# Performance work log

Measured on AMD Instinct MI355X. Metric: run time of the kernel, lower is better.

## Reference

```python
import jax, jax.numpy as jnp
import numpy as np

# convDU3 with stride=1: the torch module loops over height, slicing each row to
# an [n, c, 1, w] tensor and running Conv2d(kernel=(9,1), padding=(4,0)) + ReLU,
# then concatenating rows back along height. Because each per-row input has
# height 1 and is zero-padded to height 9, only the CENTER kernel tap W[:,:,4,0]
# multiplies real data; all other taps multiply zeros. Hence the module is
# mathematically identical to a 1x1 conv with W[:,:,4,0] + bias, then ReLU,
# applied to the full [n, c, h, w] map. We implement that fused form.

CENTER_TAP = 4  # (kernel_h - 1) // 2 for kernel_h = 9


def setup_inputs() -> dict:
    key = jax.random.key(0)
    k1, k2, k3 = jax.random.split(key, 3)
    n, c_in, h, w = 16, 2048, 32, 32
    c_out = 512
    fea = jax.random.normal(k1, (n, c_in, h, w), dtype=jnp.float32)
    # Conv2d weight [out, in, kh, kw] with kaiming-ish scale
    W = jax.random.normal(k2, (c_out, c_in, 9, 1), dtype=jnp.float32) * (1.0 / np.sqrt(c_in * 9))
    b = jax.random.normal(k3, (c_out,), dtype=jnp.float32) * 0.01
    return {"fea": fea, "W": W, "b": b}


def reference(fea, W, b):
    # Only the center tap of the (9,1) kernel contributes (zero padding elsewhere).
    Wc = W[:, :, CENTER_TAP, 0]                      # [c_out, c_in]
    out = jnp.einsum('nchw,oc->nohw', fea, Wc)       # 1x1-conv GEMM
    out = out + b[None, :, None, None]
    return jax.nn.relu(out)
```

## Files before the change

### kernel.cpp

```cpp
#include <hip/hip_runtime.h>

#define C_IN   2048
#define HWSZ   1024
#define NBATCH 16
#define C_OUT  512
#define BM 128
#define BN 128
#define BK 64
#define NKSTEP (C_IN/BK)

typedef __attribute__((ext_vector_type(4))) float f32x4;
typedef __attribute__((ext_vector_type(8))) short bf16x8;

__device__ __forceinline__ unsigned short f2bf(float x){
  unsigned int u = __float_as_uint(x);
  u += 0x7fffu + ((u >> 16) & 1u);
  return (unsigned short)(u >> 16);
}

__global__ void prep_w_kernel(const float* __restrict__ W,
                              unsigned short* __restrict__ Wh){
  int i = blockIdx.x * 256 + threadIdx.x;
  Wh[i] = f2bf(W[(size_t)i * 9 + 4]);
}

union FragU { bf16x8 v; uint4 q; };

__global__ __launch_bounds__(256, 2) void gemm_kernel(
    const float* __restrict__ fea,
    const unsigned short* __restrict__ Wh,
    const float* __restrict__ bias,
    float* __restrict__ out)
{
  __shared__ unsigned short Ah[BM*BK];
  __shared__ unsigned short Bh[BN*BK];
  __shared__ float bias_s[BM];

  const int t   = threadIdx.x;
  const int l   = t & 63;
  const int wid = t >> 6;

  const int bx  = blockIdx.x;
  const int xcd = bx & 7;
  const int s_  = bx >> 3;
  const int mt  = s_ & 3;
  const int pl  = xcd * 16 + (s_ >> 2);
  const int pt  = pl & 7;
  const int nb  = pl >> 3;

  if (t < BM) bias_s[t] = bias[mt*BM + t];

  const unsigned short* whg = Wh + (size_t)mt*BM*C_IN;
  const float* fg = fea + (size_t)nb*C_IN*HWSZ + (size_t)pt*BN;

  const int wr0 = t >> 2;
  const int wh4 = t & 3;
  const int cb  = t >> 5;
  const int pb  = t & 31;

  f32x4 acc[4][4];
  #pragma unroll
  for (int i=0;i<4;i++)
    #pragma unroll
    for (int j=0;j<4;j++) acc[i][j] = (f32x4)0.0f;

  uint4 wv[2][2];
  f32x4 fv[8];

  #pragma unroll
  for (int i=0;i<2;i++)
    #pragma unroll
    for (int h=0;h<2;h++)
      wv[i][h] = *(const uint4*)(whg + (size_t)(wr0 + i*64)*C_IN + h*32 + wh4*8);
  #pragma unroll
  for (int i=0;i<8;i++)
    fv[i] = *(const f32x4*)(fg + (size_t)(cb*8 + i)*HWSZ + pb*4);

  const int fr    = l & 15;
  const int o2    = l >> 4;
  const int mrow0 = (wid >> 1) * 64;
  const int ncol0 = (wid & 1) * 64;

  for (int ks = 0; ks < NKSTEP; ks++){
    __syncthreads();
    #pragma unroll
    for (int i=0;i<2;i++){
      const int r   = wr0 + i*64;
      const int key = (r & 7) << 1;
      #pragma unroll
      for (int h=0;h<2;h++){
        const int q0 = h*8 + wh4*2;
        *(uint4*)&Ah[r*BK + ((q0 ^ key))*4] = wv[i][h];
      }
    }
    {
      unsigned short hb[8][4];
      #pragma unroll
      for (int i=0;i<8;i++)
        #pragma unroll
        for (int j=0;j<4;j++) hb[i][j] = f2bf(fv[i][j]);
      #pragma unroll
      for (int j=0;j<4;j++){
        const int p   = pb*4 + j;
        const int key = (p & 7) << 1;
        uint4 v;
        v.x = (unsigned)hb[0][j] | ((unsigned)hb[1][j] << 16);
        v.y = (unsigned)hb[2][j] | ((unsigned)hb[3][j] << 16);
        v.z = (unsigned)hb[4][j] | ((unsigned)hb[5][j] << 16);
        v.w = (unsigned)hb[6][j] | ((unsigned)hb[7][j] << 16);
        *(uint4*)&Bh[p*BK + (((2*cb) ^ key))*4] = v;
      }
    }
    __syncthreads();

    if (ks + 1 < NKSTEP){
      const int c0 = (ks + 1) * BK;
      #pragma unroll
      for (int i=0;i<2;i++)
        #pragma unroll
        for (int h=0;h<2;h++)
          wv[i][h] = *(const uint4*)(whg + (size_t)(wr0 + i*64)*C_IN + c0 + h*32 + wh4*8);
      #pragma unroll
      for (int i=0;i<8;i++)
        fv[i] = *(const f32x4*)(fg + (size_t)(c0 + cb*8 + i)*HWSZ + pb*4);
    }

    FragU af[4][2], bff[4][2];
    #pragma unroll
    for (int mf=0; mf<4; mf++){
      const int r   = mrow0 + mf*16 + fr;
      const int key = (r & 7) << 1;
      #pragma unroll
      for (int s=0; s<2; s++)
        af[mf][s].q = *(const uint4*)&Ah[r*BK + (((s*8 + 2*o2) ^ key))*4];
    }
    #pragma unroll
    for (int nf=0; nf<4; nf++){
      const int p   = ncol0 + nf*16 + fr;
      const int key = (p & 7) << 1;
      #pragma unroll
      for (int s=0; s<2; s++)
        bff[nf][s].q = *(const uint4*)&Bh[p*BK + (((s*8 + 2*o2) ^ key))*4];
    }

    #pragma unroll
    for (int mf=0; mf<4; mf++)
      #pragma unroll
      for (int nf=0; nf<4; nf++)
        #pragma unroll
        for (int s=0; s<2; s++)
          acc[mf][nf] = __builtin_amdgcn_mfma_f32_16x16x32_bf16(af[mf][s].v, bff[nf][s].v, acc[mf][nf], 0, 0, 0);
  }

  float* ob = out + ((size_t)nb*C_OUT + mt*BM) * HWSZ + (size_t)pt*BN;
  #pragma unroll
  for (int mf=0; mf<4; mf++){
    #pragma unroll
    for (int nf=0; nf<4; nf++){
      const int p = ncol0 + nf*16 + fr;
      #pragma unroll
      for (int rr=0; rr<4; rr++){
        const int o = mrow0 + mf*16 + o2*4 + rr;
        float x = acc[mf][nf][rr] + bias_s[o];
        x = fmaxf(x, 0.0f);
        ob[(size_t)o*HWSZ + p] = x;
      }
    }
  }
}

extern "C" void kernel_launch(void* const* d_in, const int* in_sizes, int n_in,
                              void* d_out, int out_size, void* d_ws, size_t ws_size,
                              hipStream_t stream){
  const float* fea = (const float*)d_in[0];
  const float* W   = (const float*)d_in[1];
  const float* b   = (const float*)d_in[2];
  float* out = (float*)d_out;
  unsigned short* Wh = (unsigned short*)d_ws;
  prep_w_kernel<<<dim3((C_OUT*C_IN)/256), dim3(256), 0, stream>>>(W, Wh);
  gemm_kernel<<<dim3(4*8*NBATCH), dim3(256), 0, stream>>>(fea, Wh, b, out);
}
```

Measured before the change: 306.8 us.

## Pre-swizzle weights into MFMA fragment order and load A directly from global

The weight-prep kernel now writes the bf16 center-tap weights in MFMA fragment order, so each wave loads its A fragments straight from global memory with coalesced 16-byte loads instead of staging them through LDS. The GEMM block shrinks to 128 threads with a 128x64 tile, and the B tile in LDS is double-buffered so only one barrier per k-step is needed. This removes the A-side LDS writes and reads and one sync per step, at the cost of twice as many blocks, each rereading the full weight slice from L2, and fewer waves per block to hide latency.

```diff
diff --git a/kernel.cpp b/kernel.cpp
--- a/kernel.cpp
+++ b/kernel.cpp
@@ -4,9 +4,7 @@
 #define HWSZ   1024
 #define NBATCH 16
 #define C_OUT  512
-#define BM 128
-#define BN 128
-#define BK 64
+#define BK     64
 #define NKSTEP (C_IN/BK)
 
 typedef __attribute__((ext_vector_type(4))) float f32x4;
@@ -18,23 +16,38 @@
   return (unsigned short)(u >> 16);
 }
 
+union FU { bf16x8 v; uint4 q; };
+
 __global__ void prep_w_kernel(const float* __restrict__ W,
-                              unsigned short* __restrict__ Wh){
-  int i = blockIdx.x * 256 + threadIdx.x;
-  Wh[i] = f2bf(W[(size_t)i * 9 + 4]);
+                              unsigned short* __restrict__ Wf){
+  const int tid  = blockIdx.x*256 + threadIdx.x;
+  const int l    = tid & 63;
+  const int frag = tid >> 6;
+  const int mfs  = frag & 7;
+  const int ks   = (frag >> 3) & 31;
+  const int wr   = (frag >> 8) & 1;
+  const int mt   = frag >> 9;
+  const int o    = mt*128 + wr*64 + (mfs>>1)*16 + (l & 15);
+  const int c0   = ks*BK + (mfs & 1)*32 + (l>>4)*8;
+  unsigned short v[8];
+  #pragma unroll
+  for (int j=0;j<8;j++)
+    v[j] = f2bf(W[((size_t)o*C_IN + (size_t)(c0 + j))*9 + 4]);
+  uint4 pk;
+  pk.x = (unsigned)v[0] | ((unsigned)v[1] << 16);
+  pk.y = (unsigned)v[2] | ((unsigned)v[3] << 16);
+  pk.z = (unsigned)v[4] | ((unsigned)v[5] << 16);
+  pk.w = (unsigned)v[6] | ((unsigned)v[7] << 16);
+  *(uint4*)(Wf + (size_t)tid*8) = pk;
 }
 
-union FragU { bf16x8 v; uint4 q; };
-
-__global__ __launch_bounds__(256, 2) void gemm_kernel(
+__global__ __launch_bounds__(128, 2) void gemm_kernel(
     const float* __restrict__ fea,
-    const unsigned short* __restrict__ Wh,
+    const unsigned short* __restrict__ Wf,
     const float* __restrict__ bias,
     float* __restrict__ out)
 {
-  __shared__ unsigned short Ah[BM*BK];
-  __shared__ unsigned short Bh[BN*BK];
-  __shared__ float bias_s[BM];
+  __shared__ unsigned short Bs[2][64*64];
 
   const int t   = threadIdx.x;
   const int l   = t & 63;
@@ -42,21 +55,19 @@
 
   const int bx  = blockIdx.x;
   const int xcd = bx & 7;
-  const int s_  = bx >> 3;
-  const int mt  = s_ & 3;
-  const int pl  = xcd * 16 + (s_ >> 2);
-  const int pt  = pl & 7;
-  const int nb  = pl >> 3;
+  const int s7  = bx >> 3;
+  const int mt  = s7 & 3;
+  const int pnl = xcd*32 + (s7 >> 2);
+  const int pt  = pnl & 15;
+  const int nb  = pnl >> 4;
 
-  if (t < BM) bias_s[t] = bias[mt*BM + t];
+  const float* fg = fea + (size_t)nb*C_IN*HWSZ + (size_t)pt*64;
+  const unsigned short* wfg = Wf + (size_t)(mt*2 + wid)*131072;
 
-  const unsigned short* whg = Wh + (size_t)mt*BM*C_IN;
-  const float* fg = fea + (size_t)nb*C_IN*HWSZ + (size_t)pt*BN;
-
-  const int wr0 = t >> 2;
-  const int wh4 = t & 3;
-  const int cb  = t >> 5;
-  const int pb  = t & 31;
+  const int pb = t & 15;
+  const int cb = t >> 4;
+  const int fr = l & 15;
+  const int o2 = l >> 4;
 
   f32x4 acc[4][4];
   #pragma unroll
@@ -64,35 +75,13 @@
     #pragma unroll
     for (int j=0;j<4;j++) acc[i][j] = (f32x4)0.0f;
 
-  uint4 wv[2][2];
   f32x4 fv[8];
-
-  #pragma unroll
-  for (int i=0;i<2;i++)
-    #pragma unroll
-    for (int h=0;h<2;h++)
-      wv[i][h] = *(const uint4*)(whg + (size_t)(wr0 + i*64)*C_IN + h*32 + wh4*8);
   #pragma unroll
   for (int i=0;i<8;i++)
     fv[i] = *(const f32x4*)(fg + (size_t)(cb*8 + i)*HWSZ + pb*4);
 
-  const int fr    = l & 15;
-  const int o2    = l >> 4;
-  const int mrow0 = (wid >> 1) * 64;
-  const int ncol0 = (wid & 1) * 64;
-
   for (int ks = 0; ks < NKSTEP; ks++){
-    __syncthreads();
-    #pragma unroll
-    for (int i=0;i<2;i++){
-      const int r   = wr0 + i*64;
-      const int key = (r & 7) << 1;
-      #pragma unroll
-      for (int h=0;h<2;h++){
-        const int q0 = h*8 + wh4*2;
-        *(uint4*)&Ah[r*BK + ((q0 ^ key))*4] = wv[i][h];
-      }
-    }
+    const int cur = ks & 1;
     {
       unsigned short hb[8][4];
       #pragma unroll
@@ -101,69 +90,67 @@
         for (int j=0;j<4;j++) hb[i][j] = f2bf(fv[i][j]);
       #pragma unroll
       for (int j=0;j<4;j++){
-        const int p   = pb*4 + j;
-        const int key = (p & 7) << 1;
-        uint4 v;
-        v.x = (unsigned)hb[0][j] | ((unsigned)hb[1][j] << 16);
-        v.y = (unsigned)hb[2][j] | ((unsigned)hb[3][j] << 16);
-        v.z = (unsigned)hb[4][j] | ((unsigned)hb[5][j] << 16);
-        v.w = (unsigned)hb[6][j] | ((unsigned)hb[7][j] << 16);
-        *(uint4*)&Bh[p*BK + (((2*cb) ^ key))*4] = v;
+        const int p = pb*4 + j;
+        uint4 pk;
+        pk.x = (unsigned)hb[0][j] | ((unsigned)hb[1][j] << 16);
+        pk.y = (unsigned)hb[2][j] | ((unsigned)hb[3][j] << 16);
+        pk.z = (unsigned)hb[4][j] | ((unsigned)hb[5][j] << 16);
+        pk.w = (unsigned)hb[6][j] | ((unsigned)hb[7][j] << 16);
+        *(uint4*)&Bs[cur][p*64 + ((cb ^ (p & 7)) << 3)] = pk;
       }
     }
     __syncthreads();
 
+    FU af[4][2];
+    #pragma unroll
+    for (int mf=0; mf<4; mf++)
+      #pragma unroll
+      for (int s=0; s<2; s++)
+        af[mf][s].q = *(const uint4*)(wfg + (size_t)((ks*8 + mf*2 + s)*64 + l)*8);
+
+    FU bf[4][2];
+    #pragma unroll
+    for (int nf=0; nf<4; nf++){
+      const int p = nf*16 + fr;
+      #pragma unroll
+      for (int s=0; s<2; s++)
+        bf[nf][s].q = *(const uint4*)&Bs[cur][p*64 + (((s*4 + o2) ^ (p & 7)) << 3)];
+    }
+
     if (ks + 1 < NKSTEP){
-      const int c0 = (ks + 1) * BK;
-      #pragma unroll
-      for (int i=0;i<2;i++)
-        #pragma unroll
-        for (int h=0;h<2;h++)
-          wv[i][h] = *(const uint4*)(whg + (size_t)(wr0 + i*64)*C_IN + c0 + h*32 + wh4*8);
+      const int c0 = (ks + 1)*BK;
       #pragma unroll
       for (int i=0;i<8;i++)
         fv[i] = *(const f32x4*)(fg + (size_t)(c0 + cb*8 + i)*HWSZ + pb*4);
     }
 
-    FragU af[4][2], bff[4][2];
-    #pragma unroll
-    for (int mf=0; mf<4; mf++){
-      const int r   = mrow0 + mf*16 + fr;
-      const int key = (r & 7) << 1;
-      #pragma unroll
-      for (int s=0; s<2; s++)
-        af[mf][s].q = *(const uint4*)&Ah[r*BK + (((s*8 + 2*o2) ^ key))*4];
-    }
-    #pragma unroll
-    for (int nf=0; nf<4; nf++){
-      const int p   = ncol0 + nf*16 + fr;
-      const int key = (p & 7) << 1;
-      #pragma unroll
-      for (int s=0; s<2; s++)
-        bff[nf][s].q = *(const uint4*)&Bh[p*BK + (((s*8 + 2*o2) ^ key))*4];
-    }
-
     #pragma unroll
     for (int mf=0; mf<4; mf++)
       #pragma unroll
-      for (int nf=0; nf<4; nf++)
-        #pragma unroll
-        for (int s=0; s<2; s++)
-          acc[mf][nf] = __builtin_amdgcn_mfma_f32_16x16x32_bf16(af[mf][s].v, bff[nf][s].v, acc[mf][nf], 0, 0, 0);
+      for (int nf=0; nf<4; nf++){
+        acc[mf][nf] = __builtin_amdgcn_mfma_f32_16x16x32_bf16(af[mf][0].v, bf[nf][0].v, acc[mf][nf], 0, 0, 0);
+        acc[mf][nf] = __builtin_amdgcn_mfma_f32_16x16x32_bf16(af[mf][1].v, bf[nf][1].v, acc[mf][nf], 0, 0, 0);
+      }
   }
 
-  float* ob = out + ((size_t)nb*C_OUT + mt*BM) * HWSZ + (size_t)pt*BN;
+  float bv[4][4];
+  #pragma unroll
+  for (int mf=0; mf<4; mf++)
+    #pragma unroll
+    for (int rr=0; rr<4; rr++)
+      bv[mf][rr] = bias[mt*128 + wid*64 + mf*16 + o2*4 + rr];
+
+  float* ob = out + ((size_t)nb*C_OUT + mt*128)*HWSZ + (size_t)pt*64;
   #pragma unroll
   for (int mf=0; mf<4; mf++){
     #pragma unroll
     for (int nf=0; nf<4; nf++){
-      const int p = ncol0 + nf*16 + fr;
+      const int p = nf*16 + fr;
       #pragma unroll
       for (int rr=0; rr<4; rr++){
-        const int o = mrow0 + mf*16 + o2*4 + rr;
-        float x = acc[mf][nf][rr] + bias_s[o];
-        x = fmaxf(x, 0.0f);
-        ob[(size_t)o*HWSZ + p] = x;
+        const int o = wid*64 + mf*16 + o2*4 + rr;
+        float x = acc[mf][nf][rr] + bv[mf][rr];
+        ob[(size_t)o*HWSZ + p] = fmaxf(x, 0.0f);
       }
     }
   }
@@ -176,7 +163,7 @@
   const float* W   = (const float*)d_in[1];
   const float* b   = (const float*)d_in[2];
   float* out = (float*)d_out;
-  unsigned short* Wh = (unsigned short*)d_ws;
-  prep_w_kernel<<<dim3((C_OUT*C_IN)/256), dim3(256), 0, stream>>>(W, Wh);
-  gemm_kernel<<<dim3(4*8*NBATCH), dim3(256), 0, stream>>>(fea, Wh, b, out);
+  unsigned short* Wf = (unsigned short*)d_ws;
+  prep_w_kernel<<<dim3(512), dim3(256), 0, stream>>>(W, Wf);
+  gemm_kernel<<<dim3(1024), dim3(128), 0, stream>>>(fea, Wf, b, out);
 }
```

Measured after the change: 291.8 us. 4.9% less time.
